# Optimization experiments

Hardware: AMD Instinct MI355X
Metric: run time of the kernel (lower is better)

## Reference

```python
import jax, jax.numpy as jnp
import numpy as np

TOP_K = 2
NOISE_STD = 1.0
EPS = 1e-9

def setup_inputs() -> dict:
    key = jax.random.key(0)
    k1, k2, k3, k4 = jax.random.split(key, 4)
    B, S, H, E = 4, 4096, 4096, 64
    hidden_states = jax.random.normal(k1, (B, S, H), dtype=jnp.float32)
    noise = jax.random.normal(k2, (B, S, E), dtype=jnp.float32)
    lim = 1.0 / np.sqrt(H)  # torch Linear default init scale
    w_gate = jax.random.uniform(k3, (E, H), dtype=jnp.float32, minval=-lim, maxval=lim)
    w_noise = jax.random.uniform(k4, (E, H), dtype=jnp.float32, minval=-lim, maxval=lim)
    return {"hidden_states": hidden_states, "noise": noise, "w_gate": w_gate, "w_noise": w_noise}

def reference(hidden_states, noise, w_gate, w_noise):
    # Gate and noise projections: [B,S,H] x [E,H]^T -> [B,S,E]
    router_logits = jnp.einsum('bsh,eh->bse', hidden_states, w_gate)
    noise_scale = jax.nn.softplus(jnp.einsum('bsh,eh->bse', hidden_states, w_noise))
    router_logits = router_logits + noise * noise_scale * NOISE_STD
    router_probs = jax.nn.softmax(router_logits, axis=-1)
    top_k_weights, top_k_indices = jax.lax.top_k(router_probs, TOP_K)
    top_k_weights = top_k_weights / (jnp.sum(top_k_weights, axis=-1, keepdims=True) + EPS)
    # Scatter normalized weights back to dense [B,S,E] via one-hot (E is small)
    E = router_probs.shape[-1]
    gate_weights = jnp.sum(jax.nn.one_hot(top_k_indices, E, dtype=router_probs.dtype) * top_k_weights[..., None], axis=-2)
    return gate_weights, top_k_indices, router_logits
```

## Files before the change

kernel.cpp:

```cpp
#include <hip/hip_runtime.h>
#include <math.h>


typedef float   f32x4   __attribute__((ext_vector_type(4)));
typedef __bf16  bf16x8  __attribute__((ext_vector_type(8)));
typedef unsigned short ushort8 __attribute__((ext_vector_type(8)));

#define EE 64
#define E2 128
#define MT 2
#define NT 8
#define BM 32

__device__ __forceinline__ unsigned short bf16_rne(float f) {
    unsigned int u = __float_as_uint(f);
    u += 0x7fffu + ((u >> 16) & 1u);
    return (unsigned short)(u >> 16);
}
__device__ __forceinline__ float bf16_f32(unsigned short h) {
    return __uint_as_float(((unsigned int)h) << 16);
}
__device__ __forceinline__ void split3(float a, unsigned short& h1,
                                       unsigned short& h2, unsigned short& h3) {
    h1 = bf16_rne(a);
    float r  = a - bf16_f32(h1);
    h2 = bf16_rne(r);
    float r2 = r - bf16_f32(h2);
    h3 = bf16_rne(r2);
}

__global__ __launch_bounds__(256) void pack_b(
    const float* __restrict__ wg, const float* __restrict__ wn,
    unsigned short* __restrict__ bp, int Hdim)
{
    int pair = blockIdx.x * 4 + (threadIdx.x >> 6);
    int l    = threadIdx.x & 63;
    int ks   = pair >> 3;
    int nt   = pair & 7;
    int col  = nt * 16 + (l & 15);
    int k    = ks * 32 + ((l >> 4) * 8);
    const float* wrow = (col < EE) ? (wg + (size_t)col * Hdim)
                                   : (wn + (size_t)(col - EE) * Hdim);
    float4 v0 = *reinterpret_cast<const float4*>(wrow + k);
    float4 v1 = *reinterpret_cast<const float4*>(wrow + k + 4);
    float vals[8] = {v0.x, v0.y, v0.z, v0.w, v1.x, v1.y, v1.z, v1.w};
    ushort8 t1, t2, t3;
    #pragma unroll
    for (int j = 0; j < 8; ++j) {
        unsigned short a, b, c;
        split3(vals[j], a, b, c);
        t1[j] = a; t2[j] = b; t3[j] = c;
    }
    size_t base = ((size_t)(ks * 8 + nt) * 3) * 512 + (size_t)l * 8;
    *reinterpret_cast<ushort8*>(bp + base        ) = t1;
    *reinterpret_cast<ushort8*>(bp + base + 512  ) = t2;
    *reinterpret_cast<ushort8*>(bp + base + 1024 ) = t3;
}

#define MFMA(a, b, c) __builtin_amdgcn_mfma_f32_16x16x32_bf16((a), (b), (c), 0, 0, 0)

__global__ __launch_bounds__(256) void router_mfma(
    const float* __restrict__ hs,
    const float* __restrict__ noise,
    const unsigned short* __restrict__ bp,
    float* __restrict__ out_gate,
    float* __restrict__ out_idx,
    float* __restrict__ out_logits,
    int Ntok, int Hdim)
{
    __shared__ float Lred[BM][E2 + 5];

    const int tid  = threadIdx.x;
    const int lane = tid & 63;
    const int w    = tid >> 6;
    const int m0   = blockIdx.x * BM;

    const int kpw   = Hdim >> 2;
    const int steps = kpw >> 5;

    f32x4 acc[MT][NT];
    #pragma unroll
    for (int mt = 0; mt < MT; ++mt)
        #pragma unroll
        for (int nt = 0; nt < NT; ++nt)
            acc[mt][nt] = f32x4{0.f, 0.f, 0.f, 0.f};

    const float* pa[MT];
    #pragma unroll
    for (int mt = 0; mt < MT; ++mt)
        pa[mt] = hs + (size_t)(m0 + mt * 16 + (lane & 15)) * Hdim
                    + (size_t)w * kpw + ((lane >> 4) * 8);

    const unsigned short* pb = bp + (size_t)(w * steps) * 12288 + (size_t)lane * 8;

    #define LOADA(d0, d1)                                                     \
        do {                                                                  \
            _Pragma("unroll")                                                 \
            for (int mt = 0; mt < MT; ++mt) {                                 \
                d0[mt] = *reinterpret_cast<const float4*>(pa[mt]);            \
                d1[mt] = *reinterpret_cast<const float4*>(pa[mt] + 4);        \
                pa[mt] += 32;                                                 \
            }                                                                 \
        } while (0)

    #define COMPUTE(s0, s1)                                                   \
        do {                                                                  \
            bf16x8 A1[MT], A2[MT], A3[MT];                                    \
            _Pragma("unroll")                                                 \
            for (int mt = 0; mt < MT; ++mt) {                                 \
                float vals[8] = {s0[mt].x, s0[mt].y, s0[mt].z, s0[mt].w,      \
                                 s1[mt].x, s1[mt].y, s1[mt].z, s1[mt].w};     \
                ushort8 u1, u2, u3;                                           \
                _Pragma("unroll")                                             \
                for (int j = 0; j < 8; ++j) {                                 \
                    unsigned short h1, h2, h3;                                \
                    split3(vals[j], h1, h2, h3);                              \
                    u1[j] = h1; u2[j] = h2; u3[j] = h3;                       \
                }                                                             \
                A1[mt] = __builtin_bit_cast(bf16x8, u1);                      \
                A2[mt] = __builtin_bit_cast(bf16x8, u2);                      \
                A3[mt] = __builtin_bit_cast(bf16x8, u3);                      \
            }                                                                 \
            _Pragma("unroll")                                                 \
            for (int nt = 0; nt < NT; ++nt) {                                 \
                bf16x8 b1 = __builtin_bit_cast(bf16x8,                        \
                    *reinterpret_cast<const ushort8*>(pb + (nt * 3 + 0) * 512)); \
                bf16x8 b2 = __builtin_bit_cast(bf16x8,                        \
                    *reinterpret_cast<const ushort8*>(pb + (nt * 3 + 1) * 512)); \
                bf16x8 b3 = __builtin_bit_cast(bf16x8,                        \
                    *reinterpret_cast<const ushort8*>(pb + (nt * 3 + 2) * 512)); \
                _Pragma("unroll")                                             \
                for (int mt = 0; mt < MT; ++mt) {                             \
                    f32x4 c = acc[mt][nt];                                    \
                    c = MFMA(A1[mt], b1, c);                                  \
                    c = MFMA(A1[mt], b2, c);                                  \
                    c = MFMA(A2[mt], b1, c);                                  \
                    c = MFMA(A2[mt], b2, c);                                  \
                    c = MFMA(A1[mt], b3, c);                                  \
                    c = MFMA(A3[mt], b1, c);                                  \
                    acc[mt][nt] = c;                                          \
                }                                                             \
            }                                                                 \
            pb += 12288;                                                      \
        } while (0)

    float4 c0[MT], c1[MT], n0[MT], n1[MT];
    LOADA(c0, c1);
    for (int s = 0; s < steps; s += 2) {
        LOADA(n0, n1);
        COMPUTE(c0, c1);
        if (s + 2 < steps) LOADA(c0, c1);
        COMPUTE(n0, n1);
    }

    #pragma unroll
    for (int ph = 0; ph < 4; ++ph) {
        if (w == ph) {
            #pragma unroll
            for (int mt = 0; mt < MT; ++mt)
                #pragma unroll
                for (int nt = 0; nt < NT; ++nt)
                    #pragma unroll
                    for (int r = 0; r < 4; ++r) {
                        int row = mt * 16 + (lane >> 4) * 4 + r;
                        int col = nt * 16 + (lane & 15);
                        if (ph == 0) Lred[row][col]  = acc[mt][nt][r];
                        else         Lred[row][col] += acc[mt][nt][r];
                    }
        }
        __syncthreads();
    }

    if (tid < BM) {
        const int t   = tid;
        const int tok = m0 + t;
        const float* nrow = noise + (size_t)tok * EE;
        float* lrow = out_logits + (size_t)tok * EE;

        float m = -3.4e38f;
        for (int e = 0; e < EE; ++e) {
            float gv = Lred[t][e];
            float nv = Lred[t][EE + e];
            float sp = fmaxf(nv, 0.f) + log1pf(expf(-fabsf(nv)));
            float l  = fmaf(nrow[e], sp, gv);
            lrow[e]  = l;
            Lred[t][e] = l;
            m = fmaxf(m, l);
        }

        float Z = 0.f;
        float p1 = -1.f, p2 = -1.f;
        int   i1 = 0,    i2 = 0;
        for (int e = 0; e < EE; ++e) {
            float p = expf(Lred[t][e] - m);
            Z += p;
            if (p > p1)      { p2 = p1; i2 = i1; p1 = p; i1 = e; }
            else if (p > p2) { p2 = p;  i2 = e; }
        }
        float q1 = p1 / Z, q2 = p2 / Z;
        float denom = q1 + q2 + 1e-9f;
        float w1 = q1 / denom, w2 = q2 / denom;

        out_idx[(size_t)tok * 2 + 0] = (float)i1;
        out_idx[(size_t)tok * 2 + 1] = (float)i2;

        float* grow = out_gate + (size_t)tok * EE;
        for (int e = 0; e < EE; ++e)
            grow[e] = (e == i1) ? w1 : ((e == i2) ? w2 : 0.f);
    }
}

extern "C" void kernel_launch(void* const* d_in, const int* in_sizes, int n_in,
                              void* d_out, int out_size, void* d_ws, size_t ws_size,
                              hipStream_t stream) {
    const float* hs    = (const float*)d_in[0];
    const float* noise = (const float*)d_in[1];
    const float* wg    = (const float*)d_in[2];
    const float* wn    = (const float*)d_in[3];

    const int Ntok = in_sizes[1] / EE;
    const int Hdim = in_sizes[2] / EE;

    float* out_gate   = (float*)d_out;
    float* out_idx    = out_gate + (size_t)Ntok * EE;
    float* out_logits = out_idx  + (size_t)Ntok * 2;

    unsigned short* bp = (unsigned short*)d_ws;

    int pairs = (Hdim / 32) * 8;
    hipLaunchKernelGGL(pack_b, dim3(pairs / 4), dim3(256), 0, stream, wg, wn, bp, Hdim);

    hipLaunchKernelGGL(router_mfma, dim3(Ntok / BM), dim3(256), 0, stream,
                       hs, noise, bp, out_gate, out_idx, out_logits, Ntok, Hdim);
}
```

Before: 169.4 us.

## Stage packed weight tiles in LDS via async global-to-LDS loads with larger blocks

The router GEMM now uses 64-token blocks of 512 threads. Eight waves are split into four row tiles and two K halves, and each wave handles one 16-row tile instead of two. The packed bf16 weight fragments are copied into double-buffered shared memory with global_load_lds, so the waves in a block share them rather than each reading them from global memory. This cuts redundant weight traffic and halves the number of blocks. In exchange it adds two barriers per step and uses about 96KB of LDS per block, which lowers occupancy.

After: 167.3 us. No clear change (-1.2%).

```diff
diff --git a/kernel.cpp b/kernel.cpp
--- a/kernel.cpp
+++ b/kernel.cpp
@@ -8,9 +8,8 @@
 
 #define EE 64
 #define E2 128
-#define MT 2
 #define NT 8
-#define BM 32
+#define BM 64
 
 __device__ __forceinline__ unsigned short bf16_rne(float f) {
     unsigned int u = __float_as_uint(f);
@@ -27,6 +26,12 @@
     h2 = bf16_rne(r);
     float r2 = r - bf16_f32(h2);
     h3 = bf16_rne(r2);
+}
+
+__device__ __forceinline__ void gload_lds16(const void* g, void* l) {
+    __builtin_amdgcn_global_load_lds(
+        (const __attribute__((address_space(1))) void*)g,
+        (__attribute__((address_space(3))) void*)l, 16, 0, 0);
 }
 
 __global__ __launch_bounds__(256) void pack_b(
@@ -59,7 +64,7 @@
 
 #define MFMA(a, b, c) __builtin_amdgcn_mfma_f32_16x16x32_bf16((a), (b), (c), 0, 0, 0)
 
-__global__ __launch_bounds__(256) void router_mfma(
+__global__ __launch_bounds__(512) void router_mfma(
     const float* __restrict__ hs,
     const float* __restrict__ noise,
     const unsigned short* __restrict__ bp,
@@ -68,108 +73,123 @@
     float* __restrict__ out_logits,
     int Ntok, int Hdim)
 {
+    __shared__ unsigned short Bst[2][2][24 * 512];
     __shared__ float Lred[BM][E2 + 5];
 
     const int tid  = threadIdx.x;
     const int lane = tid & 63;
     const int w    = tid >> 6;
+    const int kh   = w >> 2;
+    const int mi   = w & 3;
     const int m0   = blockIdx.x * BM;
 
-    const int kpw   = Hdim >> 2;
-    const int steps = kpw >> 5;
-
-    f32x4 acc[MT][NT];
+    const int khalf = Hdim >> 1;
+    const int steps = khalf >> 5;
+
+    f32x4 acc[NT];
     #pragma unroll
-    for (int mt = 0; mt < MT; ++mt)
-        #pragma unroll
-        for (int nt = 0; nt < NT; ++nt)
-            acc[mt][nt] = f32x4{0.f, 0.f, 0.f, 0.f};
-
-    const float* pa[MT];
+    for (int nt = 0; nt < NT; ++nt) acc[nt] = f32x4{0.f, 0.f, 0.f, 0.f};
+
+    const float* pa = hs + (size_t)(m0 + mi * 16 + (lane & 15)) * Hdim
+                         + (size_t)kh * khalf + ((lane >> 4) * 8);
+
+    const unsigned short* srcB[6];
+    unsigned short* dstB[2][6];
     #pragma unroll
-    for (int mt = 0; mt < MT; ++mt)
-        pa[mt] = hs + (size_t)(m0 + mt * 16 + (lane & 15)) * Hdim
-                    + (size_t)w * kpw + ((lane >> 4) * 8);
-
-    const unsigned short* pb = bp + (size_t)(w * steps) * 12288 + (size_t)lane * 8;
+    for (int j = 0; j < 6; ++j) {
+        int c   = tid + 512 * j;
+        int ckh = c / 1536;
+        int r   = c % 1536;
+        int f   = r >> 6;
+        int l   = r & 63;
+        srcB[j]    = bp + (size_t)(ckh * steps) * 12288 + f * 512 + l * 8;
+        dstB[0][j] = &Bst[0][ckh][f * 512 + l * 8];
+        dstB[1][j] = &Bst[1][ckh][f * 512 + l * 8];
+    }
+
+    #define STAGE(buf)                                                        \
+        do {                                                                  \
+            _Pragma("unroll")                                                 \
+            for (int j = 0; j < 6; ++j) {                                     \
+                gload_lds16(srcB[j], dstB[buf][j]);                           \
+                srcB[j] += 12288;                                             \
+            }                                                                 \
+        } while (0)
 
     #define LOADA(d0, d1)                                                     \
         do {                                                                  \
+            d0 = *reinterpret_cast<const float4*>(pa);                        \
+            d1 = *reinterpret_cast<const float4*>(pa + 4);                    \
+            pa += 32;                                                         \
+        } while (0)
+
+    #define COMPUTE(s0, s1, buf)                                              \
+        do {                                                                  \
+            float vals[8] = {s0.x, s0.y, s0.z, s0.w, s1.x, s1.y, s1.z, s1.w}; \
+            ushort8 u1, u2, u3;                                               \
             _Pragma("unroll")                                                 \
-            for (int mt = 0; mt < MT; ++mt) {                                 \
-                d0[mt] = *reinterpret_cast<const float4*>(pa[mt]);            \
-                d1[mt] = *reinterpret_cast<const float4*>(pa[mt] + 4);        \
-                pa[mt] += 32;                                                 \
+            for (int j = 0; j < 8; ++j) {                                     \
+                unsigned short h1, h2, h3;                                    \
+                split3(vals[j], h1, h2, h3);                                  \
+                u1[j] = h1; u2[j] = h2; u3[j] = h3;                           \
             }                                                                 \
-        } while (0)
-
-    #define COMPUTE(s0, s1)                                                   \
-        do {                                                                  \
-            bf16x8 A1[MT], A2[MT], A3[MT];                                    \
-            _Pragma("unroll")                                                 \
-            for (int mt = 0; mt < MT; ++mt) {                                 \
-                float vals[8] = {s0[mt].x, s0[mt].y, s0[mt].z, s0[mt].w,      \
-                                 s1[mt].x, s1[mt].y, s1[mt].z, s1[mt].w};     \
-                ushort8 u1, u2, u3;                                           \
-                _Pragma("unroll")                                             \
-                for (int j = 0; j < 8; ++j) {                                 \
-                    unsigned short h1, h2, h3;                                \
-                    split3(vals[j], h1, h2, h3);                              \
-                    u1[j] = h1; u2[j] = h2; u3[j] = h3;                       \
-                }                                                             \
-                A1[mt] = __builtin_bit_cast(bf16x8, u1);                      \
-                A2[mt] = __builtin_bit_cast(bf16x8, u2);                      \
-                A3[mt] = __builtin_bit_cast(bf16x8, u3);                      \
-            }                                                                 \
+            bf16x8 A1 = __builtin_bit_cast(bf16x8, u1);                       \
+            bf16x8 A2 = __builtin_bit_cast(bf16x8, u2);                       \
+            bf16x8 A3 = __builtin_bit_cast(bf16x8, u3);                       \
+            const unsigned short* bb = &Bst[buf][kh][lane * 8];               \
             _Pragma("unroll")                                                 \
             for (int nt = 0; nt < NT; ++nt) {                                 \
                 bf16x8 b1 = __builtin_bit_cast(bf16x8,                        \
-                    *reinterpret_cast<const ushort8*>(pb + (nt * 3 + 0) * 512)); \
+                    *reinterpret_cast<const ushort8*>(bb + (nt * 3 + 0) * 512)); \
                 bf16x8 b2 = __builtin_bit_cast(bf16x8,                        \
-                    *reinterpret_cast<const ushort8*>(pb + (nt * 3 + 1) * 512)); \
+                    *reinterpret_cast<const ushort8*>(bb + (nt * 3 + 1) * 512)); \
                 bf16x8 b3 = __builtin_bit_cast(bf16x8,                        \
-                    *reinterpret_cast<const ushort8*>(pb + (nt * 3 + 2) * 512)); \
-                _Pragma("unroll")                                             \
-                for (int mt = 0; mt < MT; ++mt) {                             \
-                    f32x4 c = acc[mt][nt];                                    \
-                    c = MFMA(A1[mt], b1, c);                                  \
-                    c = MFMA(A1[mt], b2, c);                                  \
-                    c = MFMA(A2[mt], b1, c);                                  \
-                    c = MFMA(A2[mt], b2, c);                                  \
-                    c = MFMA(A1[mt], b3, c);                                  \
-                    c = MFMA(A3[mt], b1, c);                                  \
-                    acc[mt][nt] = c;                                          \
-                }                                                             \
+                    *reinterpret_cast<const ushort8*>(bb + (nt * 3 + 2) * 512)); \
+                f32x4 c = acc[nt];                                            \
+                c = MFMA(A1, b1, c);                                          \
+                c = MFMA(A1, b2, c);                                          \
+                c = MFMA(A2, b1, c);                                          \
+                c = MFMA(A2, b2, c);                                          \
+                c = MFMA(A1, b3, c);                                          \
+                c = MFMA(A3, b1, c);                                          \
+                acc[nt] = c;                                                  \
             }                                                                 \
-            pb += 12288;                                                      \
         } while (0)
 
-    float4 c0[MT], c1[MT], n0[MT], n1[MT];
+    STAGE(0);
+    float4 c0, c1, n0, n1;
     LOADA(c0, c1);
+    __syncthreads();
+
     for (int s = 0; s < steps; s += 2) {
+        STAGE(1);
         LOADA(n0, n1);
-        COMPUTE(c0, c1);
-        if (s + 2 < steps) LOADA(c0, c1);
-        COMPUTE(n0, n1);
-    }
-
-    #pragma unroll
-    for (int ph = 0; ph < 4; ++ph) {
-        if (w == ph) {
+        COMPUTE(c0, c1, 0);
+        __syncthreads();
+        if (s + 2 < steps) {
+            STAGE(0);
+            LOADA(c0, c1);
+        }
+        COMPUTE(n0, n1, 1);
+        __syncthreads();
+    }
+
+    if (kh == 0) {
+        #pragma unroll
+        for (int nt = 0; nt < NT; ++nt)
             #pragma unroll
-            for (int mt = 0; mt < MT; ++mt)
-                #pragma unroll
-                for (int nt = 0; nt < NT; ++nt)
-                    #pragma unroll
-                    for (int r = 0; r < 4; ++r) {
-                        int row = mt * 16 + (lane >> 4) * 4 + r;
-                        int col = nt * 16 + (lane & 15);
-                        if (ph == 0) Lred[row][col]  = acc[mt][nt][r];
-                        else         Lred[row][col] += acc[mt][nt][r];
-                    }
-        }
-        __syncthreads();
-    }
+            for (int r = 0; r < 4; ++r)
+                Lred[mi * 16 + (lane >> 4) * 4 + r][nt * 16 + (lane & 15)] = acc[nt][r];
+    }
+    __syncthreads();
+    if (kh == 1) {
+        #pragma unroll
+        for (int nt = 0; nt < NT; ++nt)
+            #pragma unroll
+            for (int r = 0; r < 4; ++r)
+                Lred[mi * 16 + (lane >> 4) * 4 + r][nt * 16 + (lane & 15)] += acc[nt][r];
+    }
+    __syncthreads();
 
     if (tid < BM) {
         const int t   = tid;
@@ -230,6 +250,6 @@
     int pairs = (Hdim / 32) * 8;
     hipLaunchKernelGGL(pack_b, dim3(pairs / 4), dim3(256), 0, stream, wg, wn, bp, Hdim);
 
-    hipLaunchKernelGGL(router_mfma, dim3(Ntok / BM), dim3(256), 0, stream,
+    hipLaunchKernelGGL(router_mfma, dim3(Ntok / BM), dim3(512), 0, stream,
                        hs, noise, bp, out_gate, out_idx, out_logits, Ntok, Hdim);
 }
```

## Replace split-K waves with per-wave N-tile partitioning over 64-token blocks

Applied to the files above, without the earlier changes.

The router GEMM's work split changes. Each of 8 waves now owns one 16-column output tile over the full K range, for a 64-token block. Before, 4 waves each took a quarter of K across all 128 columns, followed by a serialized LDS reduction. This removes the four-phase shared-memory reduction and cuts per-wave accumulator registers so occupancy can rise. The cost is that every wave reloads and re-splits the same hidden-state rows into three bf16 parts, which multiplies A traffic and VALU split work by 8. The split now uses native __bf16 casts and s_setprio around the MFMA bursts.

Result: slower. 290.2 us (+71.3%).

```diff
diff --git a/kernel.cpp b/kernel.cpp
--- a/kernel.cpp
+++ b/kernel.cpp
@@ -8,9 +8,8 @@
 
 #define EE 64
 #define E2 128
-#define MT 2
-#define NT 8
-#define BM 32
+#define BM 64
+#define MT 4
 
 __device__ __forceinline__ unsigned short bf16_rne(float f) {
     unsigned int u = __float_as_uint(f);
@@ -59,7 +58,7 @@
 
 #define MFMA(a, b, c) __builtin_amdgcn_mfma_f32_16x16x32_bf16((a), (b), (c), 0, 0, 0)
 
-__global__ __launch_bounds__(256) void router_mfma(
+__global__ __launch_bounds__(512, 2) void router_mfma(
     const float* __restrict__ hs,
     const float* __restrict__ noise,
     const unsigned short* __restrict__ bp,
@@ -72,26 +71,21 @@
 
     const int tid  = threadIdx.x;
     const int lane = tid & 63;
-    const int w    = tid >> 6;
+    const int nq   = tid >> 6;
     const int m0   = blockIdx.x * BM;
 
-    const int kpw   = Hdim >> 2;
-    const int steps = kpw >> 5;
-
-    f32x4 acc[MT][NT];
+    const int steps = Hdim >> 5;
+
+    f32x4 acc[MT];
     #pragma unroll
-    for (int mt = 0; mt < MT; ++mt)
-        #pragma unroll
-        for (int nt = 0; nt < NT; ++nt)
-            acc[mt][nt] = f32x4{0.f, 0.f, 0.f, 0.f};
+    for (int mt = 0; mt < MT; ++mt) acc[mt] = f32x4{0.f, 0.f, 0.f, 0.f};
 
     const float* pa[MT];
     #pragma unroll
     for (int mt = 0; mt < MT; ++mt)
-        pa[mt] = hs + (size_t)(m0 + mt * 16 + (lane & 15)) * Hdim
-                    + (size_t)w * kpw + ((lane >> 4) * 8);
-
-    const unsigned short* pb = bp + (size_t)(w * steps) * 12288 + (size_t)lane * 8;
+        pa[mt] = hs + (size_t)(m0 + mt * 16 + (lane & 15)) * Hdim + ((lane >> 4) * 8);
+
+    const unsigned short* pbw = bp + (size_t)(nq * 3) * 512 + (size_t)lane * 8;
 
     #define LOADA(d0, d1)                                                     \
         do {                                                                  \
@@ -103,73 +97,63 @@
             }                                                                 \
         } while (0)
 
-    #define COMPUTE(s0, s1)                                                   \
+    #define COMPUTE(s, s0, s1)                                                \
         do {                                                                  \
+            const unsigned short* pb = pbw + (size_t)(s) * 12288;             \
+            ushort8 bu1 = *reinterpret_cast<const ushort8*>(pb);              \
+            ushort8 bu2 = *reinterpret_cast<const ushort8*>(pb + 512);        \
+            ushort8 bu3 = *reinterpret_cast<const ushort8*>(pb + 1024);       \
             bf16x8 A1[MT], A2[MT], A3[MT];                                    \
             _Pragma("unroll")                                                 \
             for (int mt = 0; mt < MT; ++mt) {                                 \
                 float vals[8] = {s0[mt].x, s0[mt].y, s0[mt].z, s0[mt].w,      \
                                  s1[mt].x, s1[mt].y, s1[mt].z, s1[mt].w};     \
-                ushort8 u1, u2, u3;                                           \
                 _Pragma("unroll")                                             \
                 for (int j = 0; j < 8; ++j) {                                 \
-                    unsigned short h1, h2, h3;                                \
-                    split3(vals[j], h1, h2, h3);                              \
-                    u1[j] = h1; u2[j] = h2; u3[j] = h3;                       \
-                }                                                             \
-                A1[mt] = __builtin_bit_cast(bf16x8, u1);                      \
-                A2[mt] = __builtin_bit_cast(bf16x8, u2);                      \
-                A3[mt] = __builtin_bit_cast(bf16x8, u3);                      \
-            }                                                                 \
-            _Pragma("unroll")                                                 \
-            for (int nt = 0; nt < NT; ++nt) {                                 \
-                bf16x8 b1 = __builtin_bit_cast(bf16x8,                        \
-                    *reinterpret_cast<const ushort8*>(pb + (nt * 3 + 0) * 512)); \
-                bf16x8 b2 = __builtin_bit_cast(bf16x8,                        \
-                    *reinterpret_cast<const ushort8*>(pb + (nt * 3 + 1) * 512)); \
-                bf16x8 b3 = __builtin_bit_cast(bf16x8,                        \
-                    *reinterpret_cast<const ushort8*>(pb + (nt * 3 + 2) * 512)); \
-                _Pragma("unroll")                                             \
-                for (int mt = 0; mt < MT; ++mt) {                             \
-                    f32x4 c = acc[mt][nt];                                    \
-                    c = MFMA(A1[mt], b1, c);                                  \
-                    c = MFMA(A1[mt], b2, c);                                  \
-                    c = MFMA(A2[mt], b1, c);                                  \
-                    c = MFMA(A2[mt], b2, c);                                  \
-                    c = MFMA(A1[mt], b3, c);                                  \
-                    c = MFMA(A3[mt], b1, c);                                  \
-                    acc[mt][nt] = c;                                          \
+                    float a  = vals[j];                                       \
+                    __bf16 h1 = (__bf16)a;                                    \
+                    float r  = a - (float)h1;                                 \
+                    __bf16 h2 = (__bf16)r;                                    \
+                    float r2 = r - (float)h2;                                 \
+                    __bf16 h3 = (__bf16)r2;                                   \
+                    A1[mt][j] = h1; A2[mt][j] = h2; A3[mt][j] = h3;           \
                 }                                                             \
             }                                                                 \
-            pb += 12288;                                                      \
+            bf16x8 b1 = __builtin_bit_cast(bf16x8, bu1);                      \
+            bf16x8 b2 = __builtin_bit_cast(bf16x8, bu2);                      \
+            bf16x8 b3 = __builtin_bit_cast(bf16x8, bu3);                      \
+            __builtin_amdgcn_s_setprio(1);                                    \
+            _Pragma("unroll")                                                 \
+            for (int mt = 0; mt < MT; ++mt) {                                 \
+                acc[mt] = MFMA(A1[mt], b1, acc[mt]);                          \
+                acc[mt] = MFMA(A1[mt], b2, acc[mt]);                          \
+                acc[mt] = MFMA(A2[mt], b1, acc[mt]);                          \
+                acc[mt] = MFMA(A2[mt], b2, acc[mt]);                          \
+                acc[mt] = MFMA(A1[mt], b3, acc[mt]);                          \
+                acc[mt] = MFMA(A3[mt], b1, acc[mt]);                          \
+            }                                                                 \
+            __builtin_amdgcn_s_setprio(0);                                    \
         } while (0)
 
     float4 c0[MT], c1[MT], n0[MT], n1[MT];
     LOADA(c0, c1);
     for (int s = 0; s < steps; s += 2) {
         LOADA(n0, n1);
-        COMPUTE(c0, c1);
+        COMPUTE(s, c0, c1);
         if (s + 2 < steps) LOADA(c0, c1);
-        COMPUTE(n0, n1);
-    }
-
-    #pragma unroll
-    for (int ph = 0; ph < 4; ++ph) {
-        if (w == ph) {
+        COMPUTE(s + 1, n0, n1);
+    }
+
+    {
+        int row = (lane >> 4) * 4;
+        int col = nq * 16 + (lane & 15);
+        #pragma unroll
+        for (int mt = 0; mt < MT; ++mt)
             #pragma unroll
-            for (int mt = 0; mt < MT; ++mt)
-                #pragma unroll
-                for (int nt = 0; nt < NT; ++nt)
-                    #pragma unroll
-                    for (int r = 0; r < 4; ++r) {
-                        int row = mt * 16 + (lane >> 4) * 4 + r;
-                        int col = nt * 16 + (lane & 15);
-                        if (ph == 0) Lred[row][col]  = acc[mt][nt][r];
-                        else         Lred[row][col] += acc[mt][nt][r];
-                    }
-        }
-        __syncthreads();
-    }
+            for (int r = 0; r < 4; ++r)
+                Lred[mt * 16 + row + r][col] = acc[mt][r];
+    }
+    __syncthreads();
 
     if (tid < BM) {
         const int t   = tid;
@@ -230,6 +214,6 @@
     int pairs = (Hdim / 32) * 8;
     hipLaunchKernelGGL(pack_b, dim3(pairs / 4), dim3(256), 0, stream, wg, wn, bp, Hdim);
 
-    hipLaunchKernelGGL(router_mfma, dim3(Ntok / BM), dim3(256), 0, stream,
+    hipLaunchKernelGGL(router_mfma, dim3(Ntok / BM), dim3(512), 0, stream,
                        hs, noise, bp, out_gate, out_idx, out_logits, Ntok, Hdim);
 }
```
